# Performance work log

Measured on AMD Instinct MI355X. Metric: run time of the kernel, lower is better.

The kernel has to match this reference:

```python
import jax, jax.numpy as jnp
import numpy as np

H = 128
EPS = 1e-5
INFERENCE_BIAS = 0.1


def setup_inputs() -> dict:
    key = jax.random.key(0)
    ks = jax.random.split(key, 10)
    n_users, n_foods, E = 100000, 50000, 1000000
    z_user = jax.random.normal(ks[0], (n_users, H), dtype=jnp.float32)
    z_food = jax.random.normal(ks[1], (n_foods, H), dtype=jnp.float32)
    row = jax.random.randint(ks[2], (E,), 0, n_users, dtype=jnp.int64)
    col = jax.random.randint(ks[3], (E,), 0, n_foods, dtype=jnp.int64)
    # lin1: Linear(2H -> H); lin2: Linear(H -> 1)
    W1 = jax.random.normal(ks[4], (H, 2 * H), dtype=jnp.float32) * (1.0 / np.sqrt(2 * H))
    b1 = jnp.zeros((H,), dtype=jnp.float32)
    gamma = jnp.ones((H,), dtype=jnp.float32)
    beta = jnp.zeros((H,), dtype=jnp.float32)
    running_mean = jax.random.normal(ks[5], (H,), dtype=jnp.float32) * 0.1
    running_var = jnp.abs(jax.random.normal(ks[6], (H,), dtype=jnp.float32)) * 0.1 + 1.0
    W2 = jax.random.normal(ks[7], (1, H), dtype=jnp.float32) * (1.0 / np.sqrt(H))
    b2 = jnp.zeros((1,), dtype=jnp.float32)
    return {"z_user": z_user, "z_food": z_food, "row": row, "col": col,
            "W1": W1, "b1": b1, "gamma": gamma, "beta": beta,
            "running_mean": running_mean, "running_var": running_var,
            "W2": W2, "b2": b2}


def reference(z_user, z_food, row, col, W1, b1, gamma, beta,
              running_mean, running_var, W2, b2):
    # gather per-edge endpoint embeddings and concat: [E, 2H]
    z = jnp.concatenate([z_user[row], z_food[col]], axis=-1)
    h = z @ W1.T + b1                                        # [E, H]
    # BatchNorm1d in eval mode: running statistics
    h = (h - running_mean) * jax.lax.rsqrt(running_var + EPS) * gamma + beta
    h = jax.nn.relu(h)                                        # dropout is identity in eval
    out = h @ W2.T + b2                                       # [E, 1]
    return jax.nn.sigmoid((out + INFERENCE_BIAS).reshape(-1)) # [E]
```

## Files before the change

kernel.cpp:

```cpp
#include <hip/hip_runtime.h>
#include <hip/hip_bf16.h>
#include <math.h>

#define H 128
#define EPS 1e-5f
#define INF_BIAS 0.1f

typedef __attribute__((ext_vector_type(8))) short bf16x8;
typedef __attribute__((ext_vector_type(4))) float f32x4;

__device__ inline unsigned short f2bf_rne(float f) {
    unsigned u = __float_as_uint(f);
    u += 0x7fffu + ((u >> 16) & 1u);
    return (unsigned short)(u >> 16);
}
__device__ inline float bf2f(unsigned short h) {
    return __uint_as_float(((unsigned)h) << 16);
}
__device__ inline unsigned pack2(float a, float b) {
    return (unsigned)f2bf_rne(a) | ((unsigned)f2bf_rne(b) << 16);
}
__device__ inline float2 unpack2(unsigned v) {
    float2 r;
    r.x = __uint_as_float(v << 16);
    r.y = __uint_as_float(v & 0xffff0000u);
    return r;
}

__global__ void prep_kernel(
    const float* __restrict__ W1, const float* __restrict__ b1,
    const float* __restrict__ gamma, const float* __restrict__ beta,
    const float* __restrict__ rm, const float* __restrict__ rv,
    unsigned short* __restrict__ Wswz_u, unsigned short* __restrict__ Wswz_f,
    float* __restrict__ d_user)
{
    const int f    = blockIdx.x;
    const int half = f >> 4, nt = (f >> 2) & 3, kt = f & 3;
    const int t    = threadIdx.x;
    const int c    = t & 15, q = t >> 4;

    const int j  = half * 64 + (c >> 2) * 16 + nt * 4 + (c & 3);
    const float a = gamma[j] * rsqrtf(rv[j] + EPS);
    const int k0 = kt * 32 + q * 8;

    unsigned short wu[8], wf[8];
    #pragma unroll
    for (int i = 0; i < 8; ++i) {
        wu[i] = f2bf_rne(a * W1[(size_t)j * (2 * H) + k0 + i]);
        wf[i] = f2bf_rne(a * W1[(size_t)j * (2 * H) + H + k0 + i]);
    }
    const size_t dst = (size_t)f * 512 + (size_t)t * 8;
    #pragma unroll
    for (int i = 0; i < 8; ++i) { Wswz_u[dst + i] = wu[i]; Wswz_f[dst + i] = wf[i]; }

    if (kt == 0 && q == 0) d_user[j] = a * (b1[j] - rm[j]) + beta[j];
}

__global__ __launch_bounds__(256, 2) void proj_mfma(
    const float* __restrict__ z_user, const float* __restrict__ z_food,
    const unsigned short* __restrict__ Wswz_u, const unsigned short* __restrict__ Wswz_f,
    const float* __restrict__ d_user,
    unsigned short* __restrict__ U, unsigned short* __restrict__ F,
    int n_users, int n_foods, int GU, int GB)
{
    const bool userMode = (blockIdx.x < (unsigned)GU);
    const float* Z;
    const unsigned short* Wsrc;
    unsigned short* Out;
    int n, blk0, nblk;
    if (userMode) { Z = z_user; Wsrc = Wswz_u; Out = U; n = n_users; blk0 = blockIdx.x;      nblk = GU; }
    else          { Z = z_food; Wsrc = Wswz_f; Out = F; n = n_foods; blk0 = blockIdx.x - GU; nblk = GB - GU; }
    const int tiles = n >> 4;

    const int wave = threadIdx.x >> 6;
    const int lane = threadIdx.x & 63;
    const int c = lane & 15;
    const int q = lane >> 4;
    const int wg   = blk0 * 4 + wave;
    const int half = wg & 1;
    const int pair = wg >> 1;
    const int stride = nblk * 2;

    bf16x8 wf[4][4];
    #pragma unroll
    for (int nt = 0; nt < 4; ++nt)
        #pragma unroll
        for (int kt = 0; kt < 4; ++kt)
            wf[nt][kt] = *(const bf16x8*)(Wsrc + (size_t)(half * 16 + nt * 4 + kt) * 512 + lane * 8);

    f32x4 dvec[4];
    #pragma unroll
    for (int nt = 0; nt < 4; ++nt) {
        if (userMode) {
            float4 d = *(const float4*)(d_user + half * 64 + q * 16 + nt * 4);
            dvec[nt] = (f32x4){d.x, d.y, d.z, d.w};
        } else {
            dvec[nt] = (f32x4){0.f, 0.f, 0.f, 0.f};
        }
    }

    auto loadZ = [&](int t, float4 zb[8]) {
        const float* zrow = Z + (size_t)(min(t, tiles - 1) * 16 + c) * H;
        #pragma unroll
        for (int kt = 0; kt < 4; ++kt) {
            const int k0 = kt * 32 + q * 8;
            zb[2 * kt + 0] = ((const float4*)(zrow + k0))[0];
            zb[2 * kt + 1] = ((const float4*)(zrow + k0))[1];
        }
    };

    auto computeStore = [&](int t, const float4 zb[8]) {
        f32x4 acc[4];
        #pragma unroll
        for (int nt = 0; nt < 4; ++nt) acc[nt] = dvec[nt];

        #pragma unroll
        for (int kt = 0; kt < 4; ++kt) {
            float4 za = zb[2 * kt + 0];
            float4 zv = zb[2 * kt + 1];
            bf16x8 zhi, zlo;
            {
                float v[8] = {za.x, za.y, za.z, za.w, zv.x, zv.y, zv.z, zv.w};
                #pragma unroll
                for (int i = 0; i < 8; ++i) {
                    unsigned short hi = f2bf_rne(v[i]);
                    unsigned short lo = f2bf_rne(v[i] - bf2f(hi));
                    zhi[i] = (short)hi; zlo[i] = (short)lo;
                }
            }
            #pragma unroll
            for (int nt = 0; nt < 4; ++nt) {
                acc[nt] = __builtin_amdgcn_mfma_f32_16x16x32_bf16(wf[nt][kt], zhi, acc[nt], 0, 0, 0);
                acc[nt] = __builtin_amdgcn_mfma_f32_16x16x32_bf16(wf[nt][kt], zlo, acc[nt], 0, 0, 0);
            }
        }

        if (t < tiles) {
            const int r = t * 16 + c;
            unsigned short* obase = Out + (size_t)r * H + half * 64 + q * 16;
            uint4 p0, p1;
            p0.x = pack2(acc[0][0], acc[0][1]); p0.y = pack2(acc[0][2], acc[0][3]);
            p0.z = pack2(acc[1][0], acc[1][1]); p0.w = pack2(acc[1][2], acc[1][3]);
            p1.x = pack2(acc[2][0], acc[2][1]); p1.y = pack2(acc[2][2], acc[2][3]);
            p1.z = pack2(acc[3][0], acc[3][1]); p1.w = pack2(acc[3][2], acc[3][3]);
            *(uint4*)(obase)     = p0;
            *(uint4*)(obase + 8) = p1;
        }
    };

    int nIt = (tiles + stride - 1) / stride;
    nIt = (nIt + 1) & ~1;

    float4 zb0[8], zb1[8];
    int t = pair;
    loadZ(t, zb0);
    for (int it = 0; it < nIt; it += 2) {
        loadZ(t + stride, zb1);
        computeStore(t, zb0);
        if (it + 2 < nIt) loadZ(t + 2 * stride, zb0);
        computeStore(t + stride, zb1);
        t += 2 * stride;
    }
}

#define EUN 4
__global__ __launch_bounds__(256) void edge_kernel(
    const unsigned short* __restrict__ U, const unsigned short* __restrict__ F,
    const int* __restrict__ row, const int* __restrict__ col,
    const float* __restrict__ W2, const float* __restrict__ b2,
    float* __restrict__ out, int E)
{
    const int lane = threadIdx.x & 15;
    const int g  = (blockIdx.x * blockDim.x + threadIdx.x) >> 4;
    const int nG = (gridDim.x * blockDim.x) >> 4;

    const float4 w2a = ((const float4*)W2)[2 * lane];
    const float4 w2b = ((const float4*)W2)[2 * lane + 1];
    const float bias = b2[0] + INF_BIAS;

    for (int e0 = g; e0 < E; e0 += EUN * nG) {
        int iu[EUN], ifo[EUN];
        #pragma unroll
        for (int i = 0; i < EUN; ++i) {
            int e  = e0 + i * nG;
            int ec = (e < E) ? e : e0;
            iu[i]  = row[ec];
            ifo[i] = col[ec];
        }
        uint4 uv[EUN], fv[EUN];
        #pragma unroll
        for (int i = 0; i < EUN; ++i) {
            uv[i] = ((const uint4*)(U + (size_t)iu[i]  * H))[lane];
            fv[i] = ((const uint4*)(F + (size_t)ifo[i] * H))[lane];
        }
        #pragma unroll
        for (int i = 0; i < EUN; ++i) {
            float2 u0 = unpack2(uv[i].x), f0 = unpack2(fv[i].x);
            float2 u1 = unpack2(uv[i].y), f1 = unpack2(fv[i].y);
            float2 u2 = unpack2(uv[i].z), f2 = unpack2(fv[i].z);
            float2 u3 = unpack2(uv[i].w), f3 = unpack2(fv[i].w);

            float s =
                w2a.x * fmaxf(u0.x + f0.x, 0.0f) +
                w2a.y * fmaxf(u0.y + f0.y, 0.0f) +
                w2a.z * fmaxf(u1.x + f1.x, 0.0f) +
                w2a.w * fmaxf(u1.y + f1.y, 0.0f) +
                w2b.x * fmaxf(u2.x + f2.x, 0.0f) +
                w2b.y * fmaxf(u2.y + f2.y, 0.0f) +
                w2b.z * fmaxf(u3.x + f3.x, 0.0f) +
                w2b.w * fmaxf(u3.y + f3.y, 0.0f);

            s += __shfl_xor(s, 8, 16);
            s += __shfl_xor(s, 4, 16);
            s += __shfl_xor(s, 2, 16);
            s += __shfl_xor(s, 1, 16);

            const int e = e0 + i * nG;
            if (lane == 0 && e < E) {
                float x = s + bias;
                out[e] = 1.0f / (1.0f + __expf(-x));
            }
        }
    }
}

extern "C" void kernel_launch(void* const* d_in, const int* in_sizes, int n_in,
                              void* d_out, int out_size, void* d_ws, size_t ws_size,
                              hipStream_t stream) {
    const float* z_user = (const float*)d_in[0];
    const float* z_food = (const float*)d_in[1];
    const int*   row    = (const int*)d_in[2];
    const int*   col    = (const int*)d_in[3];
    const float* W1     = (const float*)d_in[4];
    const float* b1     = (const float*)d_in[5];
    const float* gamma  = (const float*)d_in[6];
    const float* beta   = (const float*)d_in[7];
    const float* rm     = (const float*)d_in[8];
    const float* rv     = (const float*)d_in[9];
    const float* W2     = (const float*)d_in[10];
    const float* b2     = (const float*)d_in[11];
    float* out = (float*)d_out;

    const int n_users = in_sizes[0] / H;
    const int n_foods = in_sizes[1] / H;
    const int E       = in_sizes[2];

    unsigned short* U      = (unsigned short*)d_ws;
    unsigned short* F      = U + (size_t)n_users * H;
    unsigned short* Wswz_u = F + (size_t)n_foods * H;
    unsigned short* Wswz_f = Wswz_u + H * H;
    float*          d_usr  = (float*)(Wswz_f + H * H);

    prep_kernel<<<32, 64, 0, stream>>>(W1, b1, gamma, beta, rm, rv,
                                       Wswz_u, Wswz_f, d_usr);

    const int GU = 342, GB = 512;
    proj_mfma<<<GB, 256, 0, stream>>>(z_user, z_food, Wswz_u, Wswz_f, d_usr,
                                      U, F, n_users, n_foods, GU, GB);

    edge_kernel<<<8192, 256, 0, stream>>>(U, F, row, col, W2, b2, out, E);
}
```

Measured before the change: 207.9 us.

## Bin edges by food index so food-embedding gathers stay cache-local

Adds a scatter kernel that buckets edges into bins of 1024 food columns using a per-block histogram and global atomic cursors, writing row, col and original edge index per bin. A new edge kernel then walks the bins so each block's food-row gathers touch a small slice of F, and it scatters the sigmoid outputs back by original edge index. The aim is better cache hit rates on the F gather. In exchange it adds an extra pass that reads and writes about 12 bytes per edge, makes the output stores scattered, and silently drops edges if a bin exceeds its fixed capacity. The binned path only runs when the workspace is large enough; otherwise the old edge kernel runs.

```diff
diff --git a/kernel.cpp b/kernel.cpp
--- a/kernel.cpp
+++ b/kernel.cpp
@@ -6,8 +6,13 @@
 #define EPS 1e-5f
 #define INF_BIAS 0.1f
 
+#define BIN_SHIFT 10
+#define CAP 24576
+#define NBMAX 64
+
 typedef __attribute__((ext_vector_type(8))) short bf16x8;
 typedef __attribute__((ext_vector_type(4))) float f32x4;
+typedef __attribute__((ext_vector_type(4))) unsigned int u32x4;
 
 __device__ inline unsigned short f2bf_rne(float f) {
     unsigned u = __float_as_uint(f);
@@ -32,12 +37,14 @@
     const float* __restrict__ gamma, const float* __restrict__ beta,
     const float* __restrict__ rm, const float* __restrict__ rv,
     unsigned short* __restrict__ Wswz_u, unsigned short* __restrict__ Wswz_f,
-    float* __restrict__ d_user)
+    float* __restrict__ d_user, int* __restrict__ binCursor, int useBinned)
 {
     const int f    = blockIdx.x;
     const int half = f >> 4, nt = (f >> 2) & 3, kt = f & 3;
     const int t    = threadIdx.x;
     const int c    = t & 15, q = t >> 4;
+
+    if (useBinned && f == 0) binCursor[t] = 0;
 
     const int j  = half * 64 + (c >> 2) * 16 + nt * 4 + (c & 3);
     const float a = gamma[j] * rsqrtf(rv[j] + EPS);
@@ -163,6 +170,107 @@
     }
 }
 
+__global__ __launch_bounds__(256) void bin_scatter(
+    const int* __restrict__ row, const int* __restrict__ col, int E,
+    int* __restrict__ binCursor,
+    int* __restrict__ br, int* __restrict__ bc, int* __restrict__ be)
+{
+    __shared__ int h[NBMAX];
+    __shared__ int cur[NBMAX];
+    const int t = threadIdx.x;
+    const int chunk = (E + gridDim.x - 1) / gridDim.x;
+    const int e0 = blockIdx.x * chunk;
+    const int e1 = min(E, e0 + chunk);
+
+    if (t < NBMAX) h[t] = 0;
+    __syncthreads();
+    for (int e = e0 + t; e < e1; e += 256)
+        atomicAdd(&h[col[e] >> BIN_SHIFT], 1);
+    __syncthreads();
+    if (t < NBMAX) {
+        const int c_ = h[t];
+        const int old = c_ ? atomicAdd(&binCursor[t], c_) : 0;
+        cur[t] = t * CAP + old;
+    }
+    __syncthreads();
+    for (int e = e0 + t; e < e1; e += 256) {
+        const int c = col[e];
+        const int b = c >> BIN_SHIFT;
+        const int pos = atomicAdd(&cur[b], 1);
+        if (pos < (b + 1) * CAP) {
+            br[pos] = row[e];
+            bc[pos] = c;
+            be[pos] = e;
+        }
+    }
+}
+
+__global__ __launch_bounds__(256) void edge_binned(
+    const unsigned short* __restrict__ U, const unsigned short* __restrict__ F,
+    const int* __restrict__ br, const int* __restrict__ bc, const int* __restrict__ be,
+    const int* __restrict__ binCursor,
+    const float* __restrict__ W2, const float* __restrict__ b2,
+    float* __restrict__ out)
+{
+    const int lane  = threadIdx.x & 15;
+    const int g     = (blockIdx.x * blockDim.x + threadIdx.x) >> 4;
+    const int slot0 = g * 4;
+    const int bin   = slot0 / CAP;
+    const int base  = bin * CAP;
+    int cnt = binCursor[bin];
+    cnt = min(cnt, CAP);
+    const int idx0 = slot0 - base;
+    if (idx0 >= cnt) return;
+
+    const float4 w2a = ((const float4*)W2)[2 * lane];
+    const float4 w2b = ((const float4*)W2)[2 * lane + 1];
+    const float bias = b2[0] + INF_BIAS;
+
+    bool act[4];
+    int iu[4], ifo[4];
+    #pragma unroll
+    for (int i = 0; i < 4; ++i) {
+        act[i] = (idx0 + i) < cnt;
+        const int s = act[i] ? (slot0 + i) : slot0;
+        iu[i]  = br[s];
+        ifo[i] = bc[s];
+    }
+    u32x4 uv[4];
+    uint4 fv[4];
+    #pragma unroll
+    for (int i = 0; i < 4; ++i) {
+        uv[i] = __builtin_nontemporal_load(((const u32x4*)(U + (size_t)iu[i] * H)) + lane);
+        fv[i] = ((const uint4*)(F + (size_t)ifo[i] * H))[lane];
+    }
+    #pragma unroll
+    for (int i = 0; i < 4; ++i) {
+        float2 u0 = unpack2(uv[i][0]), f0 = unpack2(fv[i].x);
+        float2 u1 = unpack2(uv[i][1]), f1 = unpack2(fv[i].y);
+        float2 u2 = unpack2(uv[i][2]), f2 = unpack2(fv[i].z);
+        float2 u3 = unpack2(uv[i][3]), f3 = unpack2(fv[i].w);
+
+        float s =
+            w2a.x * fmaxf(u0.x + f0.x, 0.0f) +
+            w2a.y * fmaxf(u0.y + f0.y, 0.0f) +
+            w2a.z * fmaxf(u1.x + f1.x, 0.0f) +
+            w2a.w * fmaxf(u1.y + f1.y, 0.0f) +
+            w2b.x * fmaxf(u2.x + f2.x, 0.0f) +
+            w2b.y * fmaxf(u2.y + f2.y, 0.0f) +
+            w2b.z * fmaxf(u3.x + f3.x, 0.0f) +
+            w2b.w * fmaxf(u3.y + f3.y, 0.0f);
+
+        s += __shfl_xor(s, 8, 16);
+        s += __shfl_xor(s, 4, 16);
+        s += __shfl_xor(s, 2, 16);
+        s += __shfl_xor(s, 1, 16);
+
+        if (lane == 0 && act[i]) {
+            const float x = s + bias;
+            out[be[slot0 + i]] = 1.0f / (1.0f + __expf(-x));
+        }
+    }
+}
+
 #define EUN 4
 __global__ __launch_bounds__(256) void edge_kernel(
     const unsigned short* __restrict__ U, const unsigned short* __restrict__ F,
@@ -250,13 +358,30 @@
     unsigned short* Wswz_u = F + (size_t)n_foods * H;
     unsigned short* Wswz_f = Wswz_u + H * H;
     float*          d_usr  = (float*)(Wswz_f + H * H);
+    int*            binCursor = (int*)(d_usr + H);
+    int*            br     = binCursor + NBMAX;
+
+    const int nb = (n_foods + (1 << BIN_SHIFT) - 1) >> BIN_SHIFT;
+    int* bc = br + (size_t)nb * CAP;
+    int* be = bc + (size_t)nb * CAP;
+    const size_t need = (size_t)((char*)(be + (size_t)nb * CAP) - (char*)d_ws);
+    const bool binned = (nb >= 1 && nb <= NBMAX && ws_size >= need);
 
     prep_kernel<<<32, 64, 0, stream>>>(W1, b1, gamma, beta, rm, rv,
-                                       Wswz_u, Wswz_f, d_usr);
+                                       Wswz_u, Wswz_f, d_usr,
+                                       binCursor, binned ? 1 : 0);
+
+    if (binned)
+        bin_scatter<<<512, 256, 0, stream>>>(row, col, E, binCursor, br, bc, be);
 
     const int GU = 342, GB = 512;
     proj_mfma<<<GB, 256, 0, stream>>>(z_user, z_food, Wswz_u, Wswz_f, d_usr,
                                       U, F, n_users, n_foods, GU, GB);
 
-    edge_kernel<<<8192, 256, 0, stream>>>(U, F, row, col, W2, b2, out, E);
-}
+    if (binned) {
+        edge_binned<<<nb * (CAP / 64), 256, 0, stream>>>(U, F, br, bc, be, binCursor,
+                                                         W2, b2, out);
+    } else {
+        edge_kernel<<<8192, 256, 0, stream>>>(U, F, row, col, W2, b2, out, E);
+    }
+}
```

Result: slower. 234.8 us (+13.0%).
